# Kernel optimization log

Measured on AMD Instinct MI355X. Metric: run time of the kernel, lower is better.

Reference implementation:

```python
import jax, jax.numpy as jnp
import numpy as np

SEQ = 8192
D_IN = 1024
D_OUT = 128


def setup_inputs() -> dict:
    key = jax.random.key(0)
    k0, k1, k2, k3 = jax.random.split(key, 4)
    # kaiming-normal-ish init for weights (std = sqrt(2/fan_in))
    std = np.sqrt(2.0 / D_IN).astype(np.float32)
    return {
        "x": jax.random.normal(k0, (SEQ, D_IN), dtype=jnp.float32),
        "wq": jax.random.normal(k1, (D_IN, D_OUT), dtype=jnp.float32) * std,
        "wk": jax.random.normal(k2, (D_IN, D_OUT), dtype=jnp.float32) * std,
        "wv": jax.random.normal(k3, (D_IN, D_OUT), dtype=jnp.float32) * std,
    }


def reference(x, wq, wk, wv):
    # q,k,v: [S, d_out]
    q = x @ wq
    k = x @ wk
    v = x @ wv
    scale = jnp.sqrt(jnp.asarray(D_OUT, dtype=q.dtype))
    scores = (q @ k.T) / scale          # [S, S]
    attn = jax.nn.softmax(scores, axis=-1)
    return attn @ v                      # [S, d_out]
```

## Files before the change

### kernel.cpp

```cpp
#include <hip/hip_runtime.h>
#include <cstdint>

#define SEQ    8192
#define DIN    1024
#define DOUT   128
#define NSPLIT 8
#define KVTILE 32
#define QTILE  64
#define QK_SCALE 0.1275174246f

typedef unsigned short u16;
typedef __bf16 bf16x8 __attribute__((ext_vector_type(8)));
typedef float  f32x4  __attribute__((ext_vector_type(4)));
typedef float  f32x16 __attribute__((ext_vector_type(16)));
typedef unsigned short u16x8 __attribute__((ext_vector_type(8)));
typedef unsigned short u16x4 __attribute__((ext_vector_type(4)));
typedef unsigned int u32x2 __attribute__((ext_vector_type(2)));
typedef unsigned int u32x4 __attribute__((ext_vector_type(4)));

__device__ __forceinline__ u16 bfc(float f) {
  return __builtin_bit_cast(u16, (__bf16)f);
}
__device__ __forceinline__ float bf2f(u16 u) {
  union { uint32_t u; float f; } c; c.u = ((uint32_t)u) << 16; return c.f;
}

__device__ __forceinline__ bf16x8 ldsu8(const u16* base, int byteoff) {
  return __builtin_bit_cast(bf16x8,
    *reinterpret_cast<const u16x8*>(reinterpret_cast<const char*>(base) + byteoff));
}
__device__ __forceinline__ bf16x8 glbu8(const u16* p) {
  return __builtin_bit_cast(bf16x8, *reinterpret_cast<const u16x8*>(p));
}

__device__ __forceinline__ void gload_lds16(const void* g, void* l) {
  __builtin_amdgcn_global_load_lds(
      (const __attribute__((address_space(1))) void*)g,
      (__attribute__((address_space(3))) void*)l, 16, 0, 0);
}

__global__ __launch_bounds__(256) void k_wtrans(const float* __restrict__ wq,
                                                const float* __restrict__ wk,
                                                const float* __restrict__ wv,
                                                u16* __restrict__ Wt) {
  const float* w = (blockIdx.y == 0) ? wq : (blockIdx.y == 1) ? wk : wv;
  int idx = blockIdx.x * 256 + threadIdx.x;
  int k = idx >> 7, n = idx & 127;
  Wt[(size_t)blockIdx.y * (DOUT * DIN) + (size_t)n * DIN + k] = bfc(w[idx]);
}

__global__ __launch_bounds__(256, 2) void k_gemm(const float* __restrict__ x,
                                                 const u16* __restrict__ Wt,
                                                 u16* __restrict__ Q,
                                                 u16* __restrict__ K,
                                                 u16* __restrict__ Vt) {
  __shared__ __attribute__((aligned(16))) u16 As[2][64 * 128];
  __shared__ __attribute__((aligned(16))) u16 Bs[2][96 * 128];
  const int tid  = threadIdx.x;
  const int lane = tid & 63, wave = tid >> 6;
  const int lm   = lane & 15, g = lane >> 4;
  const int wm   = wave >> 1, wn = wave & 1;
  const int m0   = blockIdx.x * 64;
  const int n0   = blockIdx.y * 96;
  const int swzr = (lm & 7) << 4;

  const int arow = tid >> 2, acol = tid & 3;
  const float* xbase = x + (size_t)(m0 + arow) * DIN + acol * 4;
  const int trow = tid >> 4;
  const int tswz = ((tid & 15) << 4) ^ ((trow & 7) << 4);
  const char* baseB = (const char*)Wt + (size_t)(n0 + trow) * 2048 + tswz;

  float4 fa[8];
  auto stage_load = [&](int bbuf, int kc) {
    const float* xp = xbase + kc * 128;
#pragma unroll
    for (int i = 0; i < 8; ++i)
      fa[i] = *reinterpret_cast<const float4*>(xp + i * 16);
    const int kb = kc * 256;
#pragma unroll
    for (int j = 0; j < 6; ++j)
      gload_lds16(baseB + kb + j * 32768, &Bs[bbuf][j * 2048 + wave * 512]);
  };
  auto stage_write = [&](int abuf) {
    char* dst = reinterpret_cast<char*>(As[abuf]) + arow * 256;
    const int sw = (arow & 7) << 4;
#pragma unroll
    for (int i = 0; i < 8; ++i) {
      u16x4 w = { bfc(fa[i].x), bfc(fa[i].y), bfc(fa[i].z), bfc(fa[i].w) };
      *reinterpret_cast<u16x4*>(dst + ((acol * 8 + i * 32) ^ sw)) = w;
    }
  };

  f32x4 acc[2][3];
#pragma unroll
  for (int s = 0; s < 2; ++s)
#pragma unroll
    for (int nb = 0; nb < 3; ++nb) acc[s][nb] = (f32x4){0.f, 0.f, 0.f, 0.f};

  auto compute = [&](int buf) {
    const u16* As_ = As[buf];
    const u16* Bs_ = Bs[buf];
    bf16x8 a[2][4], b[3][4];
#pragma unroll
    for (int s = 0; s < 2; ++s)
#pragma unroll
      for (int t = 0; t < 4; ++t)
        a[s][t] = ldsu8(As_, (wm * 32 + s * 16 + lm) * 256 +
                             ((t * 64 + 16 * g) ^ swzr));
#pragma unroll
    for (int nb = 0; nb < 3; ++nb)
#pragma unroll
      for (int t = 0; t < 4; ++t)
        b[nb][t] = ldsu8(Bs_, (wn * 48 + nb * 16 + lm) * 256 +
                              ((t * 64 + 16 * g) ^ swzr));
#pragma unroll
    for (int s = 0; s < 2; ++s)
#pragma unroll
      for (int nb = 0; nb < 3; ++nb)
#pragma unroll
        for (int t = 0; t < 4; ++t)
          acc[s][nb] = __builtin_amdgcn_mfma_f32_16x16x32_bf16(
              a[s][t], b[nb][t], acc[s][nb], 0, 0, 0);
  };

  stage_load(0, 0);
  stage_write(0);
  asm volatile("s_waitcnt vmcnt(0)" ::: "memory");
  __syncthreads();

#pragma unroll
  for (int kc = 0; kc < 8; kc += 2) {
    if (kc + 1 < 8) stage_load(1, kc + 1);
    compute(0);
    if (kc + 1 < 8) stage_write(1);
    asm volatile("s_waitcnt vmcnt(0)" ::: "memory");
    __syncthreads();
    if (kc + 2 < 8) stage_load(0, kc + 2);
    compute(1);
    if (kc + 2 < 8) stage_write(0);
    asm volatile("s_waitcnt vmcnt(0)" ::: "memory");
    __syncthreads();
  }

#pragma unroll
  for (int s = 0; s < 2; ++s)
#pragma unroll
    for (int nb = 0; nb < 3; ++nb) {
      int n = n0 + wn * 48 + nb * 16 + lm;
      int which = n >> 7, col = n & 127;
#pragma unroll
      for (int r = 0; r < 4; ++r) {
        int m = m0 + wm * 32 + s * 16 + g * 4 + r;
        if (which == 0)       Q[(size_t)m * DOUT + col] = bfc(acc[s][nb][r] * QK_SCALE);
        else if (which == 1)  K[(size_t)m * DOUT + col] = bfc(acc[s][nb][r]);
        else                  Vt[(size_t)col * SEQ + m] = bfc(acc[s][nb][r]);
      }
    }
}

__global__ __launch_bounds__(128, 2) void k_attn(const u16* __restrict__ Q,
                                                 const u16* __restrict__ K,
                                                 const u16* __restrict__ Vt,
                                                 u16* __restrict__ Op,
                                                 float* __restrict__ Lb) {
  __shared__ __attribute__((aligned(16))) u16 Ks[2][32 * 128];
  __shared__ __attribute__((aligned(16))) u16 Vts[3][128 * 32];
  const int tid  = threadIdx.x;
  const int lane = tid & 63, wave = tid >> 6;
  const int l31  = lane & 31, h = lane >> 5;
  const int bid  = blockIdx.x;
  const int split = bid & 7;
  const int m0   = (bid >> 3) * QTILE;
  const int kvbase = split * (SEQ / NSPLIT);
  const int NIT = (SEQ / NSPLIT) / KVTILE;

  auto stageK = [&](int kb, int kv0) {
#pragma unroll
    for (int i = 0; i < 4; ++i) {
      int krow = wave * 16 + i * 4 + (lane >> 4);
      const char* gk = (const char*)K + ((size_t)(kv0 + krow) << 8) +
                       (((lane & 15) << 4) ^ ((krow & 7) << 4));
      gload_lds16(gk, &Ks[kb][wave * 2048 + i * 512]);
    }
  };
  auto stageV = [&](u16* vbuf, int kv0) {
#pragma unroll
    for (int i = 0; i < 4; ++i) {
      int vrow = wave * 64 + i * 16 + (lane >> 2);
      const char* gv = (const char*)Vt + (size_t)vrow * (SEQ * 2) +
                       (size_t)kv0 * 2 +
                       (((lane & 3) << 4) ^ (((vrow >> 1) & 3) << 4));
      gload_lds16(gv, vbuf + wave * 2048 + i * 512);
    }
  };

  bf16x8 qf[8];

  f32x16 o[4] = {};
  float lr = 0.f;

  auto qk = [&](const u16* ks) -> f32x16 {
    f32x16 a0 = {}, a1 = {};
    const int rswz = (l31 & 7) << 4;
#pragma unroll
    for (int t = 0; t < 8; t += 2) {
      bf16x8 k0 = ldsu8(ks, l31 * 256 + ((t * 32 + 16 * h) ^ rswz));
      bf16x8 k1 = ldsu8(ks, l31 * 256 + (((t + 1) * 32 + 16 * h) ^ rswz));
      a0 = __builtin_amdgcn_mfma_f32_32x32x16_bf16(k0, qf[t], a0, 0, 0, 0);
      a1 = __builtin_amdgcn_mfma_f32_32x32x16_bf16(k1, qf[t + 1], a1, 0, 0, 0);
    }
    return a0 + a1;
  };

  auto smpv = [&](f32x16 s, const u16* vs) {
    float rsum = 0.f;
#pragma unroll
    for (int j = 0; j < 2; ++j) {
      const int base = j * 8;
      float e0 = exp2f(s[base + 0]);
      float e1 = exp2f(s[base + 1]);
      float e2 = exp2f(s[base + 2]);
      float e3 = exp2f(s[base + 3]);
      float e4 = exp2f(s[base + 4]);
      float e5 = exp2f(s[base + 5]);
      float e6 = exp2f(s[base + 6]);
      float e7 = exp2f(s[base + 7]);
      rsum += ((e0 + e1) + (e2 + e3)) + ((e4 + e5) + (e6 + e7));
      u16x4 wa = { bfc(e0), bfc(e1), bfc(e2), bfc(e3) };
      u16x4 wb = { bfc(e4), bfc(e5), bfc(e6), bfc(e7) };
      u32x2 A = __builtin_bit_cast(u32x2, wa);
      u32x2 B = __builtin_bit_cast(u32x2, wb);
      u32x2 r01 = __builtin_amdgcn_permlane32_swap(A.x, B.x, false, false);
      u32x2 r23 = __builtin_amdgcn_permlane32_swap(A.y, B.y, false, false);
      u32x4 fr = { r01.x, r23.x, r01.y, r23.y };
      bf16x8 pb = __builtin_bit_cast(bf16x8, fr);
#pragma unroll
      for (int db = 0; db < 4; ++db) {
        int vrow = db * 32 + l31;
        bf16x8 vb = ldsu8(vs, vrow * 64 +
                              ((32 * j + 16 * h) ^ (((vrow >> 1) & 3) << 4)));
        o[db] = __builtin_amdgcn_mfma_f32_32x32x16_bf16(vb, pb, o[db], 0, 0, 0);
      }
    }
    lr += rsum;
  };

  u16 *vA = Vts[0], *vB = Vts[1], *vC = Vts[2];
  stageK(0, kvbase);
  stageV(vA, kvbase);
  stageK(1, kvbase + KVTILE);
  stageV(vB, kvbase + KVTILE);
  {
    const u16* qp = Q + (size_t)(m0 + wave * 32 + l31) * DOUT + 8 * h;
#pragma unroll
    for (int t = 0; t < 8; ++t) qf[t] = glbu8(qp + t * 16);
  }
  asm volatile("s_waitcnt vmcnt(0)" ::: "memory");
  __syncthreads();
  f32x16 sA = qk(Ks[0]);
  f32x16 sB;

  for (int t = 0; t < NIT; t += 2) {
    const bool more = (t + 2 < NIT);
    if (more) asm volatile("s_waitcnt vmcnt(4) lgkmcnt(0)" ::: "memory");
    else      asm volatile("s_waitcnt vmcnt(0) lgkmcnt(0)" ::: "memory");
    __builtin_amdgcn_s_barrier();
    if (more) {
      stageK(0, kvbase + (t + 2) * KVTILE);
      stageV(vC, kvbase + (t + 2) * KVTILE);
    }
    sB = qk(Ks[1]);
    smpv(sA, vA);
    { u16* tp = vA; vA = vB; vB = vC; vC = tp; }

    if (more) asm volatile("s_waitcnt vmcnt(4) lgkmcnt(0)" ::: "memory");
    else      asm volatile("s_waitcnt vmcnt(0) lgkmcnt(0)" ::: "memory");
    __builtin_amdgcn_s_barrier();
    if (t + 3 < NIT) {
      stageK(1, kvbase + (t + 3) * KVTILE);
      stageV(vC, kvbase + (t + 3) * KVTILE);
    }
    if (more) sA = qk(Ks[0]);
    smpv(sB, vA);
    { u16* tp = vA; vA = vB; vB = vC; vC = tp; }
  }

  lr += __shfl_xor(lr, 32);

  const size_t ob = (size_t)split * SEQ * DOUT;
  const int q = m0 + wave * 32 + l31;
#pragma unroll
  for (int db = 0; db < 4; ++db)
#pragma unroll
    for (int j = 0; j < 4; ++j) {
      u16x4 w = { bfc(o[db][4 * j + 0]), bfc(o[db][4 * j + 1]),
                  bfc(o[db][4 * j + 2]), bfc(o[db][4 * j + 3]) };
      *reinterpret_cast<u16x4*>(Op + ob + (size_t)q * DOUT +
                                db * 32 + 8 * j + 4 * h) = w;
    }
  if (h == 0) Lb[split * SEQ + q] = lr;
}

__global__ __launch_bounds__(256) void k_combine(const u16* __restrict__ Op,
                                                 const float* __restrict__ Lb,
                                                 float* __restrict__ out) {
  int e0 = (blockIdx.x * 256 + threadIdx.x) * 8;
  int srow = e0 >> 7;
  float den = 0.f;
  float acc[8] = {};
  const size_t st = (size_t)SEQ * DOUT;
#pragma unroll
  for (int s = 0; s < NSPLIT; ++s) {
    den += Lb[s * SEQ + srow];
    u16x8 v = *reinterpret_cast<const u16x8*>(Op + s * st + e0);
#pragma unroll
    for (int i = 0; i < 8; ++i) acc[i] += bf2f(v[i]);
  }
  float r = 1.f / den;
  float4 o0 = { acc[0] * r, acc[1] * r, acc[2] * r, acc[3] * r };
  float4 o1 = { acc[4] * r, acc[5] * r, acc[6] * r, acc[7] * r };
  *reinterpret_cast<float4*>(out + e0) = o0;
  *reinterpret_cast<float4*>(out + e0 + 4) = o1;
}

extern "C" void kernel_launch(void* const* d_in, const int* in_sizes, int n_in,
                              void* d_out, int out_size, void* d_ws, size_t ws_size,
                              hipStream_t stream) {
  const float* x  = (const float*)d_in[0];
  const float* wq = (const float*)d_in[1];
  const float* wk = (const float*)d_in[2];
  const float* wv = (const float*)d_in[3];
  char* ws = (char*)d_ws;

  const size_t MB = (size_t)1 << 20;
  u16*   Wt = (u16*)(ws);
  u16*   Q  = (u16*)(ws + 768 * 1024);
  u16*   K  = (u16*)(ws + 768 * 1024 + 2 * MB);
  u16*   Vt = (u16*)(ws + 768 * 1024 + 4 * MB);
  float* Lb = (float*)(ws + 768 * 1024 + 6 * MB + 256 * 1024);
  u16*   Op = (u16*)(ws + 7 * MB + 256 * 1024);
  float* out = (float*)d_out;

  k_wtrans<<<dim3((DIN * DOUT) / 256, 3), 256, 0, stream>>>(wq, wk, wv, Wt);
  k_gemm<<<dim3(SEQ / 64, 4), 256, 0, stream>>>(x, Wt, Q, K, Vt);
  k_attn<<<dim3((SEQ / QTILE) * NSPLIT), 128, 0, stream>>>(Q, K, Vt, Op, Lb);
  k_combine<<<dim3((SEQ * DOUT) / (256 * 8)), 256, 0, stream>>>(Op, Lb, out);
}
```

Before: 86.72 us.

## Use single-wave attention blocks to drop barriers and restructure K/V staging

The attention kernel now runs one 64-thread wave per block over a 32-query tile, in place of two waves covering 64 queries. Because each block is a single wave, the workgroup barriers go away and only vmcnt waits order the LDS staging. The pipeline changes from a triple-buffered V ring to double-buffered K and V with a different prefetch distance. This doubles the block count and the total K/V traffic through LDS, since each block now reloads K and V for only half as many queries. It also raises occupancy flexibility and the LDS footprint per wave.

```diff
diff --git a/kernel.cpp b/kernel.cpp
--- a/kernel.cpp
+++ b/kernel.cpp
@@ -6,7 +6,7 @@
 #define DOUT   128
 #define NSPLIT 8
 #define KVTILE 32
-#define QTILE  64
+#define QTILE  32
 #define QK_SCALE 0.1275174246f
 
 typedef unsigned short u16;
@@ -158,15 +158,14 @@
     }
 }
 
-__global__ __launch_bounds__(128, 2) void k_attn(const u16* __restrict__ Q,
-                                                 const u16* __restrict__ K,
-                                                 const u16* __restrict__ Vt,
-                                                 u16* __restrict__ Op,
-                                                 float* __restrict__ Lb) {
+__global__ __launch_bounds__(64) void k_attn(const u16* __restrict__ Q,
+                                             const u16* __restrict__ K,
+                                             const u16* __restrict__ Vt,
+                                             u16* __restrict__ Op,
+                                             float* __restrict__ Lb) {
   __shared__ __attribute__((aligned(16))) u16 Ks[2][32 * 128];
-  __shared__ __attribute__((aligned(16))) u16 Vts[3][128 * 32];
-  const int tid  = threadIdx.x;
-  const int lane = tid & 63, wave = tid >> 6;
+  __shared__ __attribute__((aligned(16))) u16 Vs[2][128 * 32];
+  const int lane = threadIdx.x;
   const int l31  = lane & 31, h = lane >> 5;
   const int bid  = blockIdx.x;
   const int split = bid & 7;
@@ -176,25 +175,30 @@
 
   auto stageK = [&](int kb, int kv0) {
 #pragma unroll
-    for (int i = 0; i < 4; ++i) {
-      int krow = wave * 16 + i * 4 + (lane >> 4);
+    for (int i = 0; i < 8; ++i) {
+      int krow = i * 4 + (lane >> 4);
       const char* gk = (const char*)K + ((size_t)(kv0 + krow) << 8) +
                        (((lane & 15) << 4) ^ ((krow & 7) << 4));
-      gload_lds16(gk, &Ks[kb][wave * 2048 + i * 512]);
-    }
-  };
-  auto stageV = [&](u16* vbuf, int kv0) {
-#pragma unroll
-    for (int i = 0; i < 4; ++i) {
-      int vrow = wave * 64 + i * 16 + (lane >> 2);
+      gload_lds16(gk, &Ks[kb][i * 512]);
+    }
+  };
+  auto stageV = [&](int vb, int kv0) {
+#pragma unroll
+    for (int i = 0; i < 8; ++i) {
+      int vrow = i * 16 + (lane >> 2);
       const char* gv = (const char*)Vt + (size_t)vrow * (SEQ * 2) +
                        (size_t)kv0 * 2 +
                        (((lane & 3) << 4) ^ (((vrow >> 1) & 3) << 4));
-      gload_lds16(gv, vbuf + wave * 2048 + i * 512);
+      gload_lds16(gv, &Vs[vb][i * 512]);
     }
   };
 
   bf16x8 qf[8];
+  {
+    const u16* qp = Q + (size_t)(m0 + l31) * DOUT + 8 * h;
+#pragma unroll
+    for (int t = 0; t < 8; ++t) qf[t] = glbu8(qp + t * 16);
+  }
 
   f32x16 o[4] = {};
   float lr = 0.f;
@@ -245,50 +249,42 @@
     lr += rsum;
   };
 
-  u16 *vA = Vts[0], *vB = Vts[1], *vC = Vts[2];
   stageK(0, kvbase);
-  stageV(vA, kvbase);
+  stageV(0, kvbase);
   stageK(1, kvbase + KVTILE);
-  stageV(vB, kvbase + KVTILE);
-  {
-    const u16* qp = Q + (size_t)(m0 + wave * 32 + l31) * DOUT + 8 * h;
-#pragma unroll
-    for (int t = 0; t < 8; ++t) qf[t] = glbu8(qp + t * 16);
-  }
-  asm volatile("s_waitcnt vmcnt(0)" ::: "memory");
-  __syncthreads();
+  asm volatile("s_waitcnt vmcnt(16)" ::: "memory");
   f32x16 sA = qk(Ks[0]);
   f32x16 sB;
 
   for (int t = 0; t < NIT; t += 2) {
-    const bool more = (t + 2 < NIT);
-    if (more) asm volatile("s_waitcnt vmcnt(4) lgkmcnt(0)" ::: "memory");
-    else      asm volatile("s_waitcnt vmcnt(0) lgkmcnt(0)" ::: "memory");
-    __builtin_amdgcn_s_barrier();
-    if (more) {
-      stageK(0, kvbase + (t + 2) * KVTILE);
-      stageV(vC, kvbase + (t + 2) * KVTILE);
-    }
-    sB = qk(Ks[1]);
-    smpv(sA, vA);
-    { u16* tp = vA; vA = vB; vB = vC; vC = tp; }
-
-    if (more) asm volatile("s_waitcnt vmcnt(4) lgkmcnt(0)" ::: "memory");
-    else      asm volatile("s_waitcnt vmcnt(0) lgkmcnt(0)" ::: "memory");
-    __builtin_amdgcn_s_barrier();
-    if (t + 3 < NIT) {
-      stageK(1, kvbase + (t + 3) * KVTILE);
-      stageV(vC, kvbase + (t + 3) * KVTILE);
-    }
-    if (more) sA = qk(Ks[0]);
-    smpv(sB, vA);
-    { u16* tp = vA; vA = vB; vB = vC; vC = tp; }
+    {
+      const bool sk = (t + 2 < NIT);
+      const bool sv = (t + 1 < NIT);
+      if (sk) stageK(0, kvbase + (t + 2) * KVTILE);
+      if (sv) stageV(1, kvbase + (t + 1) * KVTILE);
+      if (sk & sv)      asm volatile("s_waitcnt vmcnt(16)" ::: "memory");
+      else if (sk | sv) asm volatile("s_waitcnt vmcnt(8)"  ::: "memory");
+      else              asm volatile("s_waitcnt vmcnt(0)"  ::: "memory");
+      if (t + 1 < NIT) sB = qk(Ks[1]);
+      smpv(sA, Vs[0]);
+    }
+    if (t + 1 < NIT) {
+      const bool sk = (t + 3 < NIT);
+      const bool sv = (t + 2 < NIT);
+      if (sk) stageK(1, kvbase + (t + 3) * KVTILE);
+      if (sv) stageV(0, kvbase + (t + 2) * KVTILE);
+      if (sk & sv)      asm volatile("s_waitcnt vmcnt(16)" ::: "memory");
+      else if (sk | sv) asm volatile("s_waitcnt vmcnt(8)"  ::: "memory");
+      else              asm volatile("s_waitcnt vmcnt(0)"  ::: "memory");
+      if (t + 2 < NIT) sA = qk(Ks[0]);
+      smpv(sB, Vs[1]);
+    }
   }
 
   lr += __shfl_xor(lr, 32);
 
   const size_t ob = (size_t)split * SEQ * DOUT;
-  const int q = m0 + wave * 32 + l31;
+  const int q = m0 + l31;
 #pragma unroll
   for (int db = 0; db < 4; ++db)
 #pragma unroll
@@ -343,6 +339,6 @@
 
   k_wtrans<<<dim3((DIN * DOUT) / 256, 3), 256, 0, stream>>>(wq, wk, wv, Wt);
   k_gemm<<<dim3(SEQ / 64, 4), 256, 0, stream>>>(x, Wt, Q, K, Vt);
-  k_attn<<<dim3((SEQ / QTILE) * NSPLIT), 128, 0, stream>>>(Q, K, Vt, Op, Lb);
+  k_attn<<<dim3((SEQ / QTILE) * NSPLIT), 64, 0, stream>>>(Q, K, Vt, Op, Lb);
   k_combine<<<dim3((SEQ * DOUT) / (256 * 8)), 256, 0, stream>>>(Op, Lb, out);
 }
```

Result: slower. 100.8 us (+16.3%).

## Shrink V staging to double buffer and raise attention kernel occupancy

Applied to the files above, without the earlier changes.

Replaces the triple-buffered V tiles in shared memory with two buffers and raises the launch bound from 2 to 3 blocks per SIMD, so more blocks can be resident. The K/V prefetch schedule is rebuilt around this: V for the next tile is issued one step later, and the vmcnt waits are adjusted to match. The Q fragment load is moved earlier so it overlaps the first tile loads. The cost is less prefetch lead time for V. The memory-count waits now come after the barrier rather than before it, which risks one wave reading shared tiles that another wave has not finished loading. The tighter register budget could also cause spills.

```diff
diff --git a/kernel.cpp b/kernel.cpp
--- a/kernel.cpp
+++ b/kernel.cpp
@@ -158,13 +158,13 @@
     }
 }
 
-__global__ __launch_bounds__(128, 2) void k_attn(const u16* __restrict__ Q,
+__global__ __launch_bounds__(128, 3) void k_attn(const u16* __restrict__ Q,
                                                  const u16* __restrict__ K,
                                                  const u16* __restrict__ Vt,
                                                  u16* __restrict__ Op,
                                                  float* __restrict__ Lb) {
   __shared__ __attribute__((aligned(16))) u16 Ks[2][32 * 128];
-  __shared__ __attribute__((aligned(16))) u16 Vts[3][128 * 32];
+  __shared__ __attribute__((aligned(16))) u16 Vs[2][128 * 32];
   const int tid  = threadIdx.x;
   const int lane = tid & 63, wave = tid >> 6;
   const int l31  = lane & 31, h = lane >> 5;
@@ -183,18 +183,23 @@
       gload_lds16(gk, &Ks[kb][wave * 2048 + i * 512]);
     }
   };
-  auto stageV = [&](u16* vbuf, int kv0) {
+  auto stageV = [&](int vb, int kv0) {
 #pragma unroll
     for (int i = 0; i < 4; ++i) {
       int vrow = wave * 64 + i * 16 + (lane >> 2);
       const char* gv = (const char*)Vt + (size_t)vrow * (SEQ * 2) +
                        (size_t)kv0 * 2 +
                        (((lane & 3) << 4) ^ (((vrow >> 1) & 3) << 4));
-      gload_lds16(gv, vbuf + wave * 2048 + i * 512);
+      gload_lds16(gv, &Vs[vb][wave * 2048 + i * 512]);
     }
   };
 
   bf16x8 qf[8];
+  {
+    const u16* qp = Q + (size_t)(m0 + wave * 32 + l31) * DOUT + 8 * h;
+#pragma unroll
+    for (int t = 0; t < 8; ++t) qf[t] = glbu8(qp + t * 16);
+  }
 
   f32x16 o[4] = {};
   float lr = 0.f;
@@ -245,44 +250,39 @@
     lr += rsum;
   };
 
-  u16 *vA = Vts[0], *vB = Vts[1], *vC = Vts[2];
   stageK(0, kvbase);
-  stageV(vA, kvbase);
+  stageV(0, kvbase);
   stageK(1, kvbase + KVTILE);
-  stageV(vB, kvbase + KVTILE);
-  {
-    const u16* qp = Q + (size_t)(m0 + wave * 32 + l31) * DOUT + 8 * h;
-#pragma unroll
-    for (int t = 0; t < 8; ++t) qf[t] = glbu8(qp + t * 16);
-  }
-  asm volatile("s_waitcnt vmcnt(0)" ::: "memory");
+  asm volatile("s_waitcnt vmcnt(4)" ::: "memory");
   __syncthreads();
   f32x16 sA = qk(Ks[0]);
   f32x16 sB;
 
   for (int t = 0; t < NIT; t += 2) {
-    const bool more = (t + 2 < NIT);
-    if (more) asm volatile("s_waitcnt vmcnt(4) lgkmcnt(0)" ::: "memory");
-    else      asm volatile("s_waitcnt vmcnt(0) lgkmcnt(0)" ::: "memory");
-    __builtin_amdgcn_s_barrier();
-    if (more) {
-      stageK(0, kvbase + (t + 2) * KVTILE);
-      stageV(vC, kvbase + (t + 2) * KVTILE);
-    }
-    sB = qk(Ks[1]);
-    smpv(sA, vA);
-    { u16* tp = vA; vA = vB; vB = vC; vC = tp; }
-
-    if (more) asm volatile("s_waitcnt vmcnt(4) lgkmcnt(0)" ::: "memory");
-    else      asm volatile("s_waitcnt vmcnt(0) lgkmcnt(0)" ::: "memory");
-    __builtin_amdgcn_s_barrier();
-    if (t + 3 < NIT) {
-      stageK(1, kvbase + (t + 3) * KVTILE);
-      stageV(vC, kvbase + (t + 3) * KVTILE);
-    }
-    if (more) sA = qk(Ks[0]);
-    smpv(sB, vA);
-    { u16* tp = vA; vA = vB; vB = vC; vC = tp; }
+    {
+      const bool sk = (t + 2 < NIT);
+      asm volatile("s_waitcnt lgkmcnt(0)" ::: "memory");
+      __builtin_amdgcn_s_barrier();
+      if (sk) stageK(0, kvbase + (t + 2) * KVTILE);
+      stageV(1, kvbase + (t + 1) * KVTILE);
+      if (sk) asm volatile("s_waitcnt vmcnt(8)" ::: "memory");
+      else    asm volatile("s_waitcnt vmcnt(4)" ::: "memory");
+      sB = qk(Ks[1]);
+      smpv(sA, Vs[0]);
+    }
+    {
+      const bool sk = (t + 3 < NIT);
+      const bool sv = (t + 2 < NIT);
+      asm volatile("s_waitcnt lgkmcnt(0)" ::: "memory");
+      __builtin_amdgcn_s_barrier();
+      if (sk) stageK(1, kvbase + (t + 3) * KVTILE);
+      if (sv) stageV(0, kvbase + (t + 2) * KVTILE);
+      if (sk && sv) asm volatile("s_waitcnt vmcnt(8)" ::: "memory");
+      else if (sv)  asm volatile("s_waitcnt vmcnt(4)" ::: "memory");
+      else          asm volatile("s_waitcnt vmcnt(0)" ::: "memory");
+      if (sv) sA = qk(Ks[0]);
+      smpv(sB, Vs[1]);
+    }
   }
 
   lr += __shfl_xor(lr, 32);
```

New measurement: 191.5 us. +120.8%, slower.
